# Kernel tuning notes

Measured on AMD Instinct MI355X. Metric: run time of the kernel, lower is better.

## Reference

```python
import jax, jax.numpy as jnp
import numpy as np

N_USERS = 100_000
N_ITEMS = 200_000
N_EDGES = 1_000_000
D = 64        # in_size == every layer_size
L = 3         # number of NGCF layers
B = 4096      # BPR batch
SLOPE = 0.2   # LeakyReLU negative slope
EPS = 1e-12   # F.normalize eps


def setup_inputs() -> dict:
    key = jax.random.key(0)
    ks = jax.random.split(key, 11)
    s = 1.0 / np.sqrt(D)  # xavier-ish scale
    return dict(
        user_feat=jax.random.normal(ks[0], (N_USERS, D), jnp.float32) * s,
        item_feat=jax.random.normal(ks[1], (N_ITEMS, D), jnp.float32) * s,
        W1=jax.random.normal(ks[2], (L, D, D), jnp.float32) * s,
        b1=jnp.zeros((L, D), jnp.float32),
        W2=jax.random.normal(ks[3], (L, D, D), jnp.float32) * s,
        b2=jnp.zeros((L, D), jnp.float32),
        edge_src=jax.random.randint(ks[4], (N_EDGES,), 0, N_USERS),
        edge_dst=jax.random.randint(ks[5], (N_EDGES,), 0, N_ITEMS),
        users=jax.random.randint(ks[6], (B,), 0, N_USERS),
        pos_items=jax.random.randint(ks[7], (B,), 0, N_ITEMS),
        neg_items=jax.random.randint(ks[8], (B,), 0, N_ITEMS),
    )


def _act_norm(h):
    # LeakyReLU(0.2) -> (dropout=identity, eval) -> row-wise L2 normalize
    h = jax.nn.leaky_relu(h, SLOPE)
    n = jnp.linalg.norm(h, axis=1, keepdims=True)
    return h / jnp.maximum(n, EPS)


def _ngcf_forward(user_feat, item_feat, W1, b1, W2, b2, edge_src, edge_dst):
    ones = jnp.ones((edge_src.shape[0],), user_feat.dtype)
    deg_u = jax.ops.segment_sum(ones, edge_src, num_segments=N_USERS)  # out-degree of users
    deg_i = jax.ops.segment_sum(ones, edge_dst, num_segments=N_ITEMS)  # in-degree of items
    norm = (deg_u[edge_src] * deg_i[edge_dst]) ** -0.5  # [E], same for both directions
    norm = norm[:, None]

    hu, hi = user_feat, item_feat
    u_embeds, i_embeds = [hu], [hi]
    for l in range(L):
        # per-edge elementwise product term (shared between both directions)
        p = hu[edge_src] * hi[edge_dst]            # [E, D]
        pw = p @ W2[l] + b2[l]                     # [E, D]
        # user -> item messages, summed per item
        m_i = norm * ((hu @ W1[l] + b1[l])[edge_src] + pw)
        # item -> user messages, summed per user
        m_u = norm * ((hi @ W1[l] + b1[l])[edge_dst] + pw)
        hi_new = jax.ops.segment_sum(m_i, edge_dst, num_segments=N_ITEMS)
        hu_new = jax.ops.segment_sum(m_u, edge_src, num_segments=N_USERS)
        hu, hi = _act_norm(hu_new), _act_norm(hi_new)
        u_embeds.append(hu)
        i_embeds.append(hi)

    user_embd = jnp.concatenate(u_embeds, axis=1)  # [N_USERS, D*(L+1)]
    item_embd = jnp.concatenate(i_embeds, axis=1)  # [N_ITEMS, D*(L+1)]
    return user_embd, item_embd


def reference(user_feat, item_feat, W1, b1, W2, b2,
              edge_src, edge_dst, users, pos_items, neg_items):
    user_embd, item_embd = _ngcf_forward(
        user_feat, item_feat, W1, b1, W2, b2, edge_src, edge_dst)
    return (user_embd[users], item_embd[pos_items], item_embd[neg_items])
```

## Files before the change

### kernel.cpp

```cpp
#include <hip/hip_runtime.h>

#define NU 100000
#define NI 200000
#define NE 1000000
#define NB 4096
#define CAP 16384
#define NBS 98
#define NBD 98
#define NTI (NI / 16)
#define NTU (NU / 16)

typedef __attribute__((ext_vector_type(8))) short bf16x8;
typedef __attribute__((ext_vector_type(4))) float f32x4;
typedef __attribute__((ext_vector_type(8))) unsigned short u16x8;

static __device__ __forceinline__ short f2bf(float f) {
  unsigned u = __builtin_bit_cast(unsigned, f);
  unsigned r = (u + 0x7fffu + ((u >> 16) & 1u)) >> 16;
  return (short)r;
}
static __device__ __forceinline__ float bf2f(unsigned short u) {
  return __builtin_bit_cast(float, ((unsigned)u) << 16);
}

__global__ __launch_bounds__(256) void binA_kernel(const int* __restrict__ src,
                                                   const int* __restrict__ dst,
                                                   int* __restrict__ gcur_s,
                                                   int* __restrict__ gcur_d,
                                                   int2* __restrict__ temp_s,
                                                   int2* __restrict__ temp_d) {
  __shared__ int lh[128], lbase[128], lpos[128];
  const int dir = blockIdx.x >> 9;
  const int cb = blockIdx.x & 511;
  const int lo = (int)(((long long)NE * cb) >> 9);
  const int hi = (int)(((long long)NE * (cb + 1)) >> 9);
  const int* key = dir ? dst : src;
  const int* oth = dir ? src : dst;
  int* gcur = dir ? gcur_d : gcur_s;
  int2* temp = dir ? temp_d : temp_s;
  const int shift = dir ? 11 : 10;
  const int tid = threadIdx.x;
  if (tid < 128) lh[tid] = 0;
  __syncthreads();
  for (int e = lo + tid; e < hi; e += 256) atomicAdd(&lh[key[e] >> shift], 1);
  __syncthreads();
  if (tid < 128) {
    const int c = lh[tid];
    lbase[tid] = c ? atomicAdd(&gcur[tid], c) : 0;
    lpos[tid] = 0;
  }
  __syncthreads();
  for (int e = lo + tid; e < hi; e += 256) {
    const int k = key[e];
    const int b = k >> shift;
    const int p = lbase[b] + atomicAdd(&lpos[b], 1);
    temp[(size_t)b * CAP + p] = make_int2(k, oth[e]);
  }
}

__global__ void bktscan_kernel(const int* __restrict__ gcur_s, const int* __restrict__ gcur_d,
                               int* __restrict__ bktofs_s, int* __restrict__ bktofs_d,
                               int* __restrict__ ofs_u, int* __restrict__ ofs_i) {
  const int t = threadIdx.x;
  if (t == 0) {
    int a = 0;
    for (int i = 0; i < NBS; ++i) { bktofs_s[i] = a; a += gcur_s[i]; }
    bktofs_s[NBS] = a;
    ofs_u[NU] = NE;
  }
  if (t == 1) {
    int a = 0;
    for (int i = 0; i < NBD; ++i) { bktofs_d[i] = a; a += gcur_d[i]; }
    bktofs_d[NBD] = a;
    ofs_i[NI] = NE;
  }
}

__global__ __launch_bounds__(256) void placeB_kernel(const int2* __restrict__ temp_s,
                                                     const int2* __restrict__ temp_d,
                                                     const int* __restrict__ gcur_s,
                                                     const int* __restrict__ gcur_d,
                                                     const int* __restrict__ bktofs_s,
                                                     const int* __restrict__ bktofs_d,
                                                     int* __restrict__ ofs_u, int* __restrict__ ofs_i,
                                                     float* __restrict__ rs_u, float* __restrict__ rs_i,
                                                     int* __restrict__ by_src, int* __restrict__ by_dst) {
  __shared__ int cnt[2048];
  __shared__ int exc[2048];
  __shared__ int wsum[256];
  const bool isdst = blockIdx.x >= NBS;
  const int b = isdst ? (int)blockIdx.x - NBS : (int)blockIdx.x;
  const int shift = isdst ? 11 : 10;
  const int nodelo = b << shift;
  const int n = isdst ? NI : NU;
  const int2* temp = (isdst ? temp_d : temp_s) + (size_t)b * CAP;
  const int ecnt = (isdst ? gcur_d : gcur_s)[b];
  const int bbase = (isdst ? bktofs_d : bktofs_s)[b];
  int* ofs = isdst ? ofs_i : ofs_u;
  float* rs = isdst ? rs_i : rs_u;
  int* by = isdst ? by_dst : by_src;
  const int tid = threadIdx.x;
  const int NN = 1 << shift;

  for (int j = tid; j < NN; j += 256) cnt[j] = 0;
  __syncthreads();
  for (int k = tid; k < ecnt; k += 256) atomicAdd(&cnt[temp[k].x - nodelo], 1);
  __syncthreads();
  const int per = NN >> 8;
  int s = 0;
  for (int j = 0; j < per; ++j) s += cnt[tid * per + j];
  wsum[tid] = s;
  __syncthreads();
  for (int off = 1; off < 256; off <<= 1) {
    int t2 = (tid >= off) ? wsum[tid - off] : 0;
    __syncthreads();
    wsum[tid] += t2;
    __syncthreads();
  }
  int run = wsum[tid] - s;
  for (int j = 0; j < per; ++j) {
    const int idx = tid * per + j;
    exc[idx] = run;
    run += cnt[idx];
  }
  __syncthreads();
  for (int j = tid; j < NN; j += 256) {
    const int node = nodelo + j;
    if (node < n) {
      ofs[node] = bbase + exc[j];
      const int d = cnt[j];
      rs[node] = d > 0 ? rsqrtf((float)d) : 0.f;
    }
  }
  __syncthreads();
  for (int j = tid; j < NN; j += 256) cnt[j] = exc[j];
  __syncthreads();
  for (int k = tid; k < ecnt; k += 256) {
    const int2 t2 = temp[k];
    const int p = bbase + atomicAdd(&cnt[t2.x - nodelo], 1);
    by[p] = t2.y;
  }
}

__global__ __launch_bounds__(256) void conv_kernel(const float* __restrict__ uf,
                                                   const float* __restrict__ itf,
                                                   unsigned short* __restrict__ hu,
                                                   unsigned short* __restrict__ hi) {
  int i = blockIdx.x * 256 + threadIdx.x;
  const int n4u = NU * 16;
  const float* in;
  unsigned short* outp;
  int j;
  if (i < n4u) {
    in = uf; outp = hu; j = i;
  } else if (i < n4u + NI * 16) {
    in = itf; outp = hi; j = i - n4u;
  } else return;
  float4 v = *(const float4*)&in[(size_t)j * 4];
  ushort4 o;
  o.x = (unsigned short)f2bf(v.x);
  o.y = (unsigned short)f2bf(v.y);
  o.z = (unsigned short)f2bf(v.z);
  o.w = (unsigned short)f2bf(v.w);
  *(ushort4*)&outp[(size_t)j * 4] = o;
}

__global__ __launch_bounds__(256) void layer_fused_kernel(const int* __restrict__ ofs_i,
                                                          const int* __restrict__ ofs_u,
                                                          const int* __restrict__ by_dst,
                                                          const int* __restrict__ by_src,
                                                          const float* __restrict__ rs_u,
                                                          const float* __restrict__ rs_i,
                                                          const unsigned short* __restrict__ hu,
                                                          const unsigned short* __restrict__ hi,
                                                          const float* __restrict__ W1,
                                                          const float* __restrict__ b1,
                                                          const float* __restrict__ W2,
                                                          const float* __restrict__ b2,
                                                          unsigned short* __restrict__ hi_new,
                                                          unsigned short* __restrict__ hu_new) {
  const int lane = threadIdx.x & 63;
  const int row16 = lane & 15;
  const int kg = lane >> 4;
  const int wid = (blockIdx.x * 256 + threadIdx.x) >> 6;
  const int nwaves = (gridDim.x * 256) >> 6;

  bf16x8 w1f[4][2], w2f[4][2];
#pragma unroll
  for (int nb = 0; nb < 4; ++nb)
#pragma unroll
    for (int kb = 0; kb < 2; ++kb) {
      const int n = nb * 16 + row16;
      const int k0 = kb * 32 + kg * 8;
      bf16x8 t1, t2;
#pragma unroll
      for (int j = 0; j < 8; ++j) {
        t1[j] = f2bf(W1[(k0 + j) * 64 + n]);
        t2[j] = f2bf(W2[(k0 + j) * 64 + n]);
      }
      w1f[nb][kb] = t1;
      w2f[nb][kb] = t2;
    }
  float bsum[4];
#pragma unroll
  for (int nb = 0; nb < 4; ++nb) bsum[nb] = b1[nb * 16 + row16] + b2[nb * 16 + row16];

  for (int t = wid; t < NTI + NTU; t += nwaves) {
    const bool item = t < NTI;
    const int tt = item ? t : t - NTI;
    const int* ofs = item ? ofs_i : ofs_u;
    const int* pay = item ? by_dst : by_src;
    const float* rso = item ? rs_u : rs_i;
    const float* rsw = item ? rs_i : rs_u;
    const unsigned short* hsrc = item ? hu : hi;
    const unsigned short* hold = item ? hi : hu;
    unsigned short* hnew = item ? hi_new : hu_new;
    const int r0 = tt * 16;
    const int node = r0 + row16;

    const int lo = ofs[node], hiE = ofs[node + 1];
    float a0[8] = {0.f, 0.f, 0.f, 0.f, 0.f, 0.f, 0.f, 0.f};
    float a1[8] = {0.f, 0.f, 0.f, 0.f, 0.f, 0.f, 0.f, 0.f};
    float cs = 0.f;
    for (int i = lo;; ++i) {
      const bool act = i < hiE;
      if (!__any(act)) break;
      if (act) {
        const int nb = pay[i];
        const float ww = rso[nb];
        const u16x8 h0 = *(const u16x8*)(hsrc + (size_t)nb * 64 + kg * 8);
        const u16x8 h1 = *(const u16x8*)(hsrc + (size_t)nb * 64 + kg * 8 + 32);
#pragma unroll
        for (int j = 0; j < 8; ++j) {
          a0[j] += ww * bf2f(h0[j]);
          a1[j] += ww * bf2f(h1[j]);
        }
        cs += ww;
      }
    }
    const float rsn = rsw[node];
    const u16x8 hv0 = *(const u16x8*)(hold + (size_t)node * 64 + kg * 8);
    const u16x8 hv1 = *(const u16x8*)(hold + (size_t)node * 64 + kg * 8 + 32);
    bf16x8 ag[2], ap[2];
#pragma unroll
    for (int j = 0; j < 8; ++j) {
      const float g0 = a0[j] * rsn;
      const float g1 = a1[j] * rsn;
      ag[0][j] = f2bf(g0);
      ag[1][j] = f2bf(g1);
      ap[0][j] = f2bf(g0 * bf2f(hv0[j]));
      ap[1][j] = f2bf(g1 * bf2f(hv1[j]));
    }
    const float csc = cs * rsn;

    f32x4 acc[4];
#pragma unroll
    for (int nb = 0; nb < 4; ++nb) acc[nb] = (f32x4){0.f, 0.f, 0.f, 0.f};
#pragma unroll
    for (int nb = 0; nb < 4; ++nb)
#pragma unroll
      for (int kb = 0; kb < 2; ++kb) {
        acc[nb] = __builtin_amdgcn_mfma_f32_16x16x32_bf16(ag[kb], w1f[nb][kb], acc[nb], 0, 0, 0);
        acc[nb] = __builtin_amdgcn_mfma_f32_16x16x32_bf16(ap[kb], w2f[nb][kb], acc[nb], 0, 0, 0);
      }
    float cv[4];
#pragma unroll
    for (int reg = 0; reg < 4; ++reg) cv[reg] = __shfl(csc, kg * 4 + reg);
    float v[4][4];
    float ss[4] = {0.f, 0.f, 0.f, 0.f};
#pragma unroll
    for (int nb = 0; nb < 4; ++nb)
#pragma unroll
      for (int reg = 0; reg < 4; ++reg) {
        float x = acc[nb][reg] + cv[reg] * bsum[nb];
        x = (x > 0.f) ? x : 0.2f * x;
        v[nb][reg] = x;
        ss[reg] += x * x;
      }
#pragma unroll
    for (int m = 1; m < 16; m <<= 1)
#pragma unroll
      for (int reg = 0; reg < 4; ++reg) ss[reg] += __shfl_xor(ss[reg], m);
    float inv[4];
#pragma unroll
    for (int reg = 0; reg < 4; ++reg) inv[reg] = 1.0f / fmaxf(sqrtf(ss[reg]), 1e-12f);
#pragma unroll
    for (int reg = 0; reg < 4; ++reg) {
      const size_t rowbase = (size_t)(r0 + kg * 4 + reg) * 64;
#pragma unroll
      for (int nb = 0; nb < 4; ++nb)
        hnew[rowbase + nb * 16 + row16] = (unsigned short)f2bf(v[nb][reg] * inv[reg]);
    }
  }
}

__global__ __launch_bounds__(256) void gather_f32_kernel(const float* __restrict__ hu,
                                                         const float* __restrict__ hi,
                                                         const int* __restrict__ users,
                                                         const int* __restrict__ pos,
                                                         const int* __restrict__ neg,
                                                         float* __restrict__ out) {
  int t = blockIdx.x * 256 + threadIdx.x;
  if (t >= 3 * NB * 64) return;
  int j = t & 63;
  int b = (t >> 6) & (NB - 1);
  int which = t / (NB * 64);
  int row = (which == 0) ? users[b] : ((which == 1) ? pos[b] : neg[b]);
  const float* h = (which == 0) ? hu : hi;
  out[(size_t)which * NB * 256 + (size_t)b * 256 + j] = h[(size_t)row * 64 + j];
}

__global__ __launch_bounds__(256) void gather_bf_kernel(const unsigned short* __restrict__ hu,
                                                        const unsigned short* __restrict__ hi,
                                                        const int* __restrict__ users,
                                                        const int* __restrict__ pos,
                                                        const int* __restrict__ neg,
                                                        float* __restrict__ out, int stage) {
  int t = blockIdx.x * 256 + threadIdx.x;
  if (t >= 3 * NB * 64) return;
  int j = t & 63;
  int b = (t >> 6) & (NB - 1);
  int which = t / (NB * 64);
  int row = (which == 0) ? users[b] : ((which == 1) ? pos[b] : neg[b]);
  const unsigned short* h = (which == 0) ? hu : hi;
  out[(size_t)which * NB * 256 + (size_t)b * 256 + (size_t)stage * 64 + j] =
      bf2f(h[(size_t)row * 64 + j]);
}

extern "C" void kernel_launch(void* const* d_in, const int* in_sizes, int n_in,
                              void* d_out, int out_size, void* d_ws, size_t ws_size,
                              hipStream_t stream) {
  (void)in_sizes; (void)n_in; (void)out_size; (void)ws_size;
  const float* user_feat = (const float*)d_in[0];
  const float* item_feat = (const float*)d_in[1];
  const float* W1 = (const float*)d_in[2];
  const float* b1 = (const float*)d_in[3];
  const float* W2 = (const float*)d_in[4];
  const float* b2 = (const float*)d_in[5];
  const int* edge_src = (const int*)d_in[6];
  const int* edge_dst = (const int*)d_in[7];
  const int* users = (const int*)d_in[8];
  const int* pos_items = (const int*)d_in[9];
  const int* neg_items = (const int*)d_in[10];
  float* out = (float*)d_out;

  char* base = (char*)d_ws;
  size_t ofsz = 0;
  auto alloc = [&](size_t bytes) -> char* {
    char* r = base + ofsz;
    ofsz += (bytes + 1023) & ~(size_t)1023;
    return r;
  };
  int* ofs_u = (int*)alloc((NU + 1) * 4);
  int* ofs_i = (int*)alloc((NI + 1) * 4);
  int* gcur_s = (int*)alloc(128 * 4);
  int* gcur_d = (int*)alloc(128 * 4);
  int* bktofs_s = (int*)alloc(128 * 4);
  int* bktofs_d = (int*)alloc(128 * 4);
  int2* temp_s = (int2*)alloc((size_t)NBS * CAP * 8);
  int2* temp_d = (int2*)alloc((size_t)NBD * CAP * 8);
  int* by_src = (int*)alloc((size_t)NE * 4);
  int* by_dst = (int*)alloc((size_t)NE * 4);
  float* rs_u = (float*)alloc((size_t)NU * 4);
  float* rs_i = (float*)alloc((size_t)NI * 4);
  unsigned short* hbU0 = (unsigned short*)alloc((size_t)NU * 64 * 2);
  unsigned short* hbU1 = (unsigned short*)alloc((size_t)NU * 64 * 2);
  unsigned short* hbI0 = (unsigned short*)alloc((size_t)NI * 64 * 2);
  unsigned short* hbI1 = (unsigned short*)alloc((size_t)NI * 64 * 2);

  unsigned short* bufU[2] = {hbU1, hbU0};
  unsigned short* bufI[2] = {hbI1, hbI0};

  hipMemsetAsync(gcur_s, 0, 128 * 4, stream);
  hipMemsetAsync(gcur_d, 0, 128 * 4, stream);
  binA_kernel<<<1024, 256, 0, stream>>>(edge_src, edge_dst, gcur_s, gcur_d, temp_s, temp_d);
  bktscan_kernel<<<1, 64, 0, stream>>>(gcur_s, gcur_d, bktofs_s, bktofs_d, ofs_u, ofs_i);
  placeB_kernel<<<NBS + NBD, 256, 0, stream>>>(temp_s, temp_d, gcur_s, gcur_d,
                                               bktofs_s, bktofs_d, ofs_u, ofs_i,
                                               rs_u, rs_i, by_src, by_dst);

  conv_kernel<<<((NU + NI) * 16 + 255) / 256, 256, 0, stream>>>(user_feat, item_feat, hbU0, hbI0);

  gather_f32_kernel<<<(3 * NB * 64 + 255) / 256, 256, 0, stream>>>(
      user_feat, item_feat, users, pos_items, neg_items, out);

  const unsigned short* hu = hbU0;
  const unsigned short* hi = hbI0;
  for (int l = 0; l < 3; ++l) {
    unsigned short* hu_new = bufU[l & 1];
    unsigned short* hi_new = bufI[l & 1];
    layer_fused_kernel<<<1024, 256, 0, stream>>>(ofs_i, ofs_u, by_dst, by_src,
                                                 rs_u, rs_i, hu, hi,
                                                 W1 + l * 4096, b1 + l * 64,
                                                 W2 + l * 4096, b2 + l * 64,
                                                 hi_new, hu_new);
    gather_bf_kernel<<<(3 * NB * 64 + 255) / 256, 256, 0, stream>>>(
        hu_new, hi_new, users, pos_items, neg_items, out, l + 1);
    hu = hu_new;
    hi = hi_new;
  }
}
```

Before: 426.9 us.

## Pre-scale embeddings by rsqrt degree and batch neighbor gathers four at a time

```diff
diff --git a/kernel.cpp b/kernel.cpp
--- a/kernel.cpp
+++ b/kernel.cpp
@@ -142,27 +142,57 @@
   }
 }
 
+__global__ __launch_bounds__(256) void c_kernel(const int* __restrict__ ofs_i,
+                                                const int* __restrict__ ofs_u,
+                                                const int* __restrict__ by_dst,
+                                                const int* __restrict__ by_src,
+                                                const float* __restrict__ rs_u,
+                                                const float* __restrict__ rs_i,
+                                                float* __restrict__ c_i,
+                                                float* __restrict__ c_u) {
+  int r = blockIdx.x * 256 + threadIdx.x;
+  if (r < NI) {
+    const int lo = ofs_i[r], hi = ofs_i[r + 1];
+    float s = 0.f;
+    for (int k = lo; k < hi; ++k) s += rs_u[by_dst[k]];
+    c_i[r] = rs_i[r] * s;
+  } else if (r < NI + NU) {
+    r -= NI;
+    const int lo = ofs_u[r], hi = ofs_u[r + 1];
+    float s = 0.f;
+    for (int k = lo; k < hi; ++k) s += rs_i[by_src[k]];
+    c_u[r] = rs_u[r] * s;
+  }
+}
+
 __global__ __launch_bounds__(256) void conv_kernel(const float* __restrict__ uf,
                                                    const float* __restrict__ itf,
+                                                   const float* __restrict__ rs_u,
+                                                   const float* __restrict__ rs_i,
                                                    unsigned short* __restrict__ hu,
-                                                   unsigned short* __restrict__ hi) {
+                                                   unsigned short* __restrict__ hi,
+                                                   unsigned short* __restrict__ hsu,
+                                                   unsigned short* __restrict__ hsi) {
   int i = blockIdx.x * 256 + threadIdx.x;
   const int n4u = NU * 16;
   const float* in;
-  unsigned short* outp;
+  const float* rs;
+  unsigned short *outp, *outs;
   int j;
   if (i < n4u) {
-    in = uf; outp = hu; j = i;
+    in = uf; rs = rs_u; outp = hu; outs = hsu; j = i;
   } else if (i < n4u + NI * 16) {
-    in = itf; outp = hi; j = i - n4u;
+    in = itf; rs = rs_i; outp = hi; outs = hsi; j = i - n4u;
   } else return;
+  const float rsn = rs[j >> 4];
   float4 v = *(const float4*)&in[(size_t)j * 4];
-  ushort4 o;
-  o.x = (unsigned short)f2bf(v.x);
-  o.y = (unsigned short)f2bf(v.y);
-  o.z = (unsigned short)f2bf(v.z);
-  o.w = (unsigned short)f2bf(v.w);
+  ushort4 o, os;
+  o.x = (unsigned short)f2bf(v.x);  os.x = (unsigned short)f2bf(v.x * rsn);
+  o.y = (unsigned short)f2bf(v.y);  os.y = (unsigned short)f2bf(v.y * rsn);
+  o.z = (unsigned short)f2bf(v.z);  os.z = (unsigned short)f2bf(v.z * rsn);
+  o.w = (unsigned short)f2bf(v.w);  os.w = (unsigned short)f2bf(v.w * rsn);
   *(ushort4*)&outp[(size_t)j * 4] = o;
+  *(ushort4*)&outs[(size_t)j * 4] = os;
 }
 
 __global__ __launch_bounds__(256) void layer_fused_kernel(const int* __restrict__ ofs_i,
@@ -171,76 +201,97 @@
                                                           const int* __restrict__ by_src,
                                                           const float* __restrict__ rs_u,
                                                           const float* __restrict__ rs_i,
+                                                          const float* __restrict__ c_i,
+                                                          const float* __restrict__ c_u,
                                                           const unsigned short* __restrict__ hu,
                                                           const unsigned short* __restrict__ hi,
+                                                          const unsigned short* __restrict__ hsu,
+                                                          const unsigned short* __restrict__ hsi,
                                                           const float* __restrict__ W1,
                                                           const float* __restrict__ b1,
                                                           const float* __restrict__ W2,
                                                           const float* __restrict__ b2,
                                                           unsigned short* __restrict__ hi_new,
-                                                          unsigned short* __restrict__ hu_new) {
-  const int lane = threadIdx.x & 63;
+                                                          unsigned short* __restrict__ hu_new,
+                                                          unsigned short* __restrict__ hsi_new,
+                                                          unsigned short* __restrict__ hsu_new) {
+  __shared__ unsigned short wlds[8192];
+  const int tid = threadIdx.x;
+  const int lane = tid & 63;
   const int row16 = lane & 15;
   const int kg = lane >> 4;
-  const int wid = (blockIdx.x * 256 + threadIdx.x) >> 6;
+  for (int ch = tid; ch < 1024; ch += 256) {
+    const int w = ch >> 9;
+    const int rem = ch & 511;
+    const int nb = rem >> 7, kb = (rem >> 6) & 1, l2 = rem & 63;
+    const int r16 = l2 & 15, kg2 = l2 >> 4;
+    const float* W = w ? W2 : W1;
+    unsigned short* dst = &wlds[ch * 8];
+#pragma unroll
+    for (int j = 0; j < 8; ++j)
+      dst[j] = (unsigned short)f2bf(W[(kb * 32 + kg2 * 8 + j) * 64 + nb * 16 + r16]);
+  }
+  __syncthreads();
+
+  float bsum[4];
+#pragma unroll
+  for (int nb = 0; nb < 4; ++nb) bsum[nb] = b1[nb * 16 + row16] + b2[nb * 16 + row16];
+
+  const int wid = (blockIdx.x * 256 + tid) >> 6;
   const int nwaves = (gridDim.x * 256) >> 6;
-
-  bf16x8 w1f[4][2], w2f[4][2];
-#pragma unroll
-  for (int nb = 0; nb < 4; ++nb)
-#pragma unroll
-    for (int kb = 0; kb < 2; ++kb) {
-      const int n = nb * 16 + row16;
-      const int k0 = kb * 32 + kg * 8;
-      bf16x8 t1, t2;
-#pragma unroll
-      for (int j = 0; j < 8; ++j) {
-        t1[j] = f2bf(W1[(k0 + j) * 64 + n]);
-        t2[j] = f2bf(W2[(k0 + j) * 64 + n]);
-      }
-      w1f[nb][kb] = t1;
-      w2f[nb][kb] = t2;
-    }
-  float bsum[4];
-#pragma unroll
-  for (int nb = 0; nb < 4; ++nb) bsum[nb] = b1[nb * 16 + row16] + b2[nb * 16 + row16];
 
   for (int t = wid; t < NTI + NTU; t += nwaves) {
     const bool item = t < NTI;
     const int tt = item ? t : t - NTI;
     const int* ofs = item ? ofs_i : ofs_u;
     const int* pay = item ? by_dst : by_src;
-    const float* rso = item ? rs_u : rs_i;
     const float* rsw = item ? rs_i : rs_u;
-    const unsigned short* hsrc = item ? hu : hi;
+    const float* cc = item ? c_i : c_u;
+    const unsigned short* hs = item ? hsu : hsi;
     const unsigned short* hold = item ? hi : hu;
     unsigned short* hnew = item ? hi_new : hu_new;
+    unsigned short* hsnew = item ? hsi_new : hsu_new;
     const int r0 = tt * 16;
     const int node = r0 + row16;
 
     const int lo = ofs[node], hiE = ofs[node + 1];
+    int rounds = (hiE - lo + 3) >> 2;
+#pragma unroll
+    for (int m = 1; m < 16; m <<= 1) rounds = max(rounds, __shfl_xor(rounds, m));
+
     float a0[8] = {0.f, 0.f, 0.f, 0.f, 0.f, 0.f, 0.f, 0.f};
     float a1[8] = {0.f, 0.f, 0.f, 0.f, 0.f, 0.f, 0.f, 0.f};
-    float cs = 0.f;
-    for (int i = lo;; ++i) {
-      const bool act = i < hiE;
-      if (!__any(act)) break;
-      if (act) {
-        const int nb = pay[i];
-        const float ww = rso[nb];
-        const u16x8 h0 = *(const u16x8*)(hsrc + (size_t)nb * 64 + kg * 8);
-        const u16x8 h1 = *(const u16x8*)(hsrc + (size_t)nb * 64 + kg * 8 + 32);
+    for (int rd = 0; rd < rounds; ++rd) {
+      const int i0 = lo + rd * 4;
+      int nb4[4];
+      float wt[4];
+#pragma unroll
+      for (int s = 0; s < 4; ++s) {
+        const int idx = i0 + s;
+        nb4[s] = pay[min(idx, NE - 1)];
+        wt[s] = (idx < hiE) ? 1.f : 0.f;
+      }
+      u16x8 h0[4], h1[4];
+#pragma unroll
+      for (int s = 0; s < 4; ++s) {
+        const unsigned short* hp = hs + (size_t)nb4[s] * 64 + kg * 8;
+        h0[s] = *(const u16x8*)hp;
+        h1[s] = *(const u16x8*)(hp + 32);
+      }
+#pragma unroll
+      for (int s = 0; s < 4; ++s)
 #pragma unroll
         for (int j = 0; j < 8; ++j) {
-          a0[j] += ww * bf2f(h0[j]);
-          a1[j] += ww * bf2f(h1[j]);
+          a0[j] += wt[s] * bf2f(h0[s][j]);
+          a1[j] += wt[s] * bf2f(h1[s][j]);
         }
-        cs += ww;
-      }
     }
+
     const float rsn = rsw[node];
-    const u16x8 hv0 = *(const u16x8*)(hold + (size_t)node * 64 + kg * 8);
-    const u16x8 hv1 = *(const u16x8*)(hold + (size_t)node * 64 + kg * 8 + 32);
+    const float cnode = cc[node];
+    const unsigned short* hp0 = hold + (size_t)node * 64 + kg * 8;
+    const u16x8 hv0 = *(const u16x8*)hp0;
+    const u16x8 hv1 = *(const u16x8*)(hp0 + 32);
     bf16x8 ag[2], ap[2];
 #pragma unroll
     for (int j = 0; j < 8; ++j) {
@@ -251,21 +302,27 @@
       ap[0][j] = f2bf(g0 * bf2f(hv0[j]));
       ap[1][j] = f2bf(g1 * bf2f(hv1[j]));
     }
-    const float csc = cs * rsn;
 
     f32x4 acc[4];
 #pragma unroll
     for (int nb = 0; nb < 4; ++nb) acc[nb] = (f32x4){0.f, 0.f, 0.f, 0.f};
+    const unsigned short* wl = wlds + lane * 8;
 #pragma unroll
     for (int nb = 0; nb < 4; ++nb)
 #pragma unroll
       for (int kb = 0; kb < 2; ++kb) {
-        acc[nb] = __builtin_amdgcn_mfma_f32_16x16x32_bf16(ag[kb], w1f[nb][kb], acc[nb], 0, 0, 0);
-        acc[nb] = __builtin_amdgcn_mfma_f32_16x16x32_bf16(ap[kb], w2f[nb][kb], acc[nb], 0, 0, 0);
+        const bf16x8 w1f = *(const bf16x8*)(wl + ((0 * 4 + nb) * 2 + kb) * 512);
+        const bf16x8 w2f = *(const bf16x8*)(wl + ((1 * 4 + nb) * 2 + kb) * 512);
+        acc[nb] = __builtin_amdgcn_mfma_f32_16x16x32_bf16(ag[kb], w1f, acc[nb], 0, 0, 0);
+        acc[nb] = __builtin_amdgcn_mfma_f32_16x16x32_bf16(ap[kb], w2f, acc[nb], 0, 0, 0);
       }
-    float cv[4];
-#pragma unroll
-    for (int reg = 0; reg < 4; ++reg) cv[reg] = __shfl(csc, kg * 4 + reg);
+
+    float cv[4], rsrow[4];
+#pragma unroll
+    for (int reg = 0; reg < 4; ++reg) {
+      cv[reg] = __shfl(cnode, kg * 4 + reg);
+      rsrow[reg] = __shfl(rsn, kg * 4 + reg);
+    }
     float v[4][4];
     float ss[4] = {0.f, 0.f, 0.f, 0.f};
 #pragma unroll
@@ -281,15 +338,17 @@
     for (int m = 1; m < 16; m <<= 1)
 #pragma unroll
       for (int reg = 0; reg < 4; ++reg) ss[reg] += __shfl_xor(ss[reg], m);
-    float inv[4];
-#pragma unroll
-    for (int reg = 0; reg < 4; ++reg) inv[reg] = 1.0f / fmaxf(sqrtf(ss[reg]), 1e-12f);
 #pragma unroll
     for (int reg = 0; reg < 4; ++reg) {
+      const float inv = 1.0f / fmaxf(sqrtf(ss[reg]), 1e-12f);
+      const float invs = inv * rsrow[reg];
       const size_t rowbase = (size_t)(r0 + kg * 4 + reg) * 64;
 #pragma unroll
-      for (int nb = 0; nb < 4; ++nb)
-        hnew[rowbase + nb * 16 + row16] = (unsigned short)f2bf(v[nb][reg] * inv[reg]);
+      for (int nb = 0; nb < 4; ++nb) {
+        const float y = v[nb][reg];
+        hnew[rowbase + nb * 16 + row16] = (unsigned short)f2bf(y * inv);
+        hsnew[rowbase + nb * 16 + row16] = (unsigned short)f2bf(y * invs);
+      }
     }
   }
 }
@@ -363,13 +422,21 @@
   int* by_dst = (int*)alloc((size_t)NE * 4);
   float* rs_u = (float*)alloc((size_t)NU * 4);
   float* rs_i = (float*)alloc((size_t)NI * 4);
+  float* c_u = (float*)alloc((size_t)NU * 4);
+  float* c_i = (float*)alloc((size_t)NI * 4);
   unsigned short* hbU0 = (unsigned short*)alloc((size_t)NU * 64 * 2);
   unsigned short* hbU1 = (unsigned short*)alloc((size_t)NU * 64 * 2);
   unsigned short* hbI0 = (unsigned short*)alloc((size_t)NI * 64 * 2);
   unsigned short* hbI1 = (unsigned short*)alloc((size_t)NI * 64 * 2);
+  unsigned short* hsU0 = (unsigned short*)alloc((size_t)NU * 64 * 2);
+  unsigned short* hsU1 = (unsigned short*)alloc((size_t)NU * 64 * 2);
+  unsigned short* hsI0 = (unsigned short*)alloc((size_t)NI * 64 * 2);
+  unsigned short* hsI1 = (unsigned short*)alloc((size_t)NI * 64 * 2);
 
   unsigned short* bufU[2] = {hbU1, hbU0};
   unsigned short* bufI[2] = {hbI1, hbI0};
+  unsigned short* bufSU[2] = {hsU1, hsU0};
+  unsigned short* bufSI[2] = {hsI1, hsI0};
 
   hipMemsetAsync(gcur_s, 0, 128 * 4, stream);
   hipMemsetAsync(gcur_d, 0, 128 * 4, stream);
@@ -378,25 +445,34 @@
   placeB_kernel<<<NBS + NBD, 256, 0, stream>>>(temp_s, temp_d, gcur_s, gcur_d,
                                                bktofs_s, bktofs_d, ofs_u, ofs_i,
                                                rs_u, rs_i, by_src, by_dst);
-
-  conv_kernel<<<((NU + NI) * 16 + 255) / 256, 256, 0, stream>>>(user_feat, item_feat, hbU0, hbI0);
+  c_kernel<<<(NI + NU + 255) / 256, 256, 0, stream>>>(ofs_i, ofs_u, by_dst, by_src,
+                                                      rs_u, rs_i, c_i, c_u);
+  conv_kernel<<<((NU + NI) * 16 + 255) / 256, 256, 0, stream>>>(
+      user_feat, item_feat, rs_u, rs_i, hbU0, hbI0, hsU0, hsI0);
 
   gather_f32_kernel<<<(3 * NB * 64 + 255) / 256, 256, 0, stream>>>(
       user_feat, item_feat, users, pos_items, neg_items, out);
 
   const unsigned short* hu = hbU0;
   const unsigned short* hi = hbI0;
+  const unsigned short* hsu = hsU0;
+  const unsigned short* hsi = hsI0;
   for (int l = 0; l < 3; ++l) {
     unsigned short* hu_new = bufU[l & 1];
     unsigned short* hi_new = bufI[l & 1];
-    layer_fused_kernel<<<1024, 256, 0, stream>>>(ofs_i, ofs_u, by_dst, by_src,
-                                                 rs_u, rs_i, hu, hi,
+    unsigned short* hsu_new = bufSU[l & 1];
+    unsigned short* hsi_new = bufSI[l & 1];
+    layer_fused_kernel<<<2048, 256, 0, stream>>>(ofs_i, ofs_u, by_dst, by_src,
+                                                 rs_u, rs_i, c_i, c_u,
+                                                 hu, hi, hsu, hsi,
                                                  W1 + l * 4096, b1 + l * 64,
                                                  W2 + l * 4096, b2 + l * 64,
-                                                 hi_new, hu_new);
+                                                 hi_new, hu_new, hsi_new, hsu_new);
     gather_bf_kernel<<<(3 * NB * 64 + 255) / 256, 256, 0, stream>>>(
         hu_new, hi_new, users, pos_items, neg_items, out, l + 1);
     hu = hu_new;
     hi = hi_new;
-  }
-}
+    hsu = hsu_new;
+    hsi = hsi_new;
+  }
+}
```

After: 435.0 us. About the same (+1.9%).
